# Optimization experiments

Measured on AMD Instinct MI355X. Metric: run time of the kernel, lower is better.

The kernel has to match this reference:

```python
import jax, jax.numpy as jnp
import numpy as np

N = 94  # nodes per graph (pinned by fc = Linear(94, 6400))


def setup_inputs() -> dict:
    key = jax.random.key(0)
    ks = jax.random.split(key, 9)
    B, E = 16384, 1504
    feature = jax.random.normal(ks[0], (B, N, 3), jnp.float32)
    edge_index = jax.random.randint(ks[1], (2, E), 0, N, jnp.int32)
    edge_weight = jax.random.uniform(ks[2], (E,), jnp.float32)
    # GCNConv weights are [in, out] (PyG applies x @ W)
    W1 = jax.random.normal(ks[3], (3, 6), jnp.float32) * 0.5
    b1 = jax.random.normal(ks[4], (6,), jnp.float32) * 0.1
    W2 = jax.random.normal(ks[5], (6, 1), jnp.float32) * 0.5
    b2 = jax.random.normal(ks[6], (1,), jnp.float32) * 0.1
    # nn.Linear stores weight as [out, in]
    Wfc = jax.random.normal(ks[7], (6400, 94), jnp.float32) * 0.1
    bfc = jax.random.normal(ks[8], (6400,), jnp.float32) * 0.1
    return dict(feature=feature, edge_index=edge_index, edge_weight=edge_weight,
                W1=W1, b1=b1, W2=W2, b2=b2, Wfc=Wfc, bfc=bfc)


def _gcn_norm(edge_index, edge_weight):
    # add self-loops with weight 1.0 (PyG default), symmetric normalization
    loops = jnp.arange(N, dtype=edge_index.dtype)
    src = jnp.concatenate([edge_index[0], loops])
    dst = jnp.concatenate([edge_index[1], loops])
    ew = jnp.concatenate([edge_weight, jnp.ones((N,), edge_weight.dtype)])
    deg = jnp.zeros((N,), edge_weight.dtype).at[dst].add(ew)
    dinv = jnp.where(deg > 0, jax.lax.rsqrt(deg), 0.0)
    norm = dinv[src] * ew * dinv[dst]  # [E+N]
    return src, dst, norm


def _gcn_conv(x, W, b, src, dst, norm):
    # x: [B, N, Cin] -> [B, N, Cout]
    xw = x @ W  # [B, N, Cout]
    msgs = xw[:, src, :] * norm[None, :, None]  # gather + scale, [B, E', Cout]
    out = jnp.zeros((x.shape[0], N, W.shape[1]), x.dtype).at[:, dst].add(msgs)
    return out + b


def reference(feature, edge_index, edge_weight, W1, b1, W2, b2, Wfc, bfc):
    src, dst, norm = _gcn_norm(edge_index, edge_weight)
    h = jnp.tanh(_gcn_conv(feature, W1, b1, src, dst, norm))  # [B, N, 6]
    h = jnp.tanh(_gcn_conv(h, W2, b2, src, dst, norm))        # [B, N, 1]
    h = h[..., 0]                                             # squeeze -> [B, N]
    return h @ Wfc.T + bfc                                    # [B, 6400]
```

## Files before the change

### kernel.cpp

```cpp
#include <hip/hip_runtime.h>
#include <hip/hip_bf16.h>
#include <cstddef>

#define NND 94
#define NPAD 96

typedef __attribute__((ext_vector_type(8))) short sh8;
typedef __attribute__((ext_vector_type(4))) float f4v;

__device__ __forceinline__ float ftanh(float x) {
    float e = __expf(2.0f * x);
    return 1.0f - 2.0f / (e + 1.0f);
}

__global__ void k_prep_adj(const int* __restrict__ ei, const float* __restrict__ ew,
                           float* __restrict__ At, int E) {
    __shared__ float deg[NPAD];
    __shared__ float dinv[NPAD];
    int tid = threadIdx.x;
    for (int i = tid; i < NPAD * NPAD; i += blockDim.x) At[i] = 0.0f;
    if (tid < NPAD) deg[tid] = 0.0f;
    __syncthreads();
    for (int e = tid; e < E; e += blockDim.x)
        atomicAdd(&deg[ei[E + e]], ew[e]);
    __syncthreads();
    if (tid < NND) {
        float d = deg[tid] + 1.0f;
        dinv[tid] = d > 0.0f ? rsqrtf(d) : 0.0f;
    }
    __syncthreads();
    for (int e = tid; e < E; e += blockDim.x) {
        int s = ei[e], d = ei[E + e];
        atomicAdd(&At[s * NPAD + d], dinv[s] * ew[e] * dinv[d]);
    }
    if (tid < NND)
        atomicAdd(&At[tid * NPAD + tid], dinv[tid] * dinv[tid]);
}

__global__ void k_pack_w(const float* __restrict__ Wfc, __hip_bfloat16* __restrict__ wp_hi,
                         __hip_bfloat16* __restrict__ wp_lo, int NOUT) {
    int t = blockIdx.x * blockDim.x + threadIdx.x;
    int total = (NOUT / 16) * 3 * 64;
    if (t >= total) return;
    int lane = t & 63;
    int kb = (t >> 6) % 3;
    int ntile = t / 192;
    int n = ntile * 16 + (lane & 15);
    int kbase = kb * 32 + ((lane >> 4) << 3);
    size_t obase = (size_t)t * 8;
#pragma unroll
    for (int j = 0; j < 8; ++j) {
        int k = kbase + j;
        float v = (k < NND) ? Wfc[(size_t)n * NND + k] : 0.0f;
        __hip_bfloat16 h = __float2bfloat16(v);
        float rem = v - __bfloat162float(h);
        wp_hi[obase + j] = h;
        wp_lo[obase + j] = __float2bfloat16(rem);
    }
}

#define K1_THREADS 512
#define NR 12

__global__ void __launch_bounds__(K1_THREADS) k_gcn(
    const float* __restrict__ feat, const float* __restrict__ W1,
    const float* __restrict__ b1, const float* __restrict__ W2,
    const float* __restrict__ b2p, const float* __restrict__ At,
    __hip_bfloat16* __restrict__ h2p) {
    extern __shared__ float lds[];
    float* xs = lds;
    float* zs = lds + 282 * 64;

    int tid = threadIdx.x;
    int lane = tid & 63;
    int g = __builtin_amdgcn_readfirstlane(tid >> 6);
    int b0 = blockIdx.x * 64;

    float w1[3][6], bb1[6], w2[6];
#pragma unroll
    for (int k = 0; k < 3; ++k)
#pragma unroll
        for (int c = 0; c < 6; ++c) w1[k][c] = W1[k * 6 + c];
#pragma unroll
    for (int c = 0; c < 6; ++c) { bb1[c] = b1[c]; w2[c] = W2[c]; }
    float b2 = b2p[0];

    for (int i = tid; i < 282 * 64; i += K1_THREADS) {
        int bl = i & 63;
        int idx = i >> 6;
        xs[idx * 64 + bl] = feat[(size_t)(b0 + bl) * 282 + idx];
    }
    __syncthreads();

    int nb = g * NR;

    float y[NR][3];
#pragma unroll
    for (int i = 0; i < NR; ++i)
#pragma unroll
        for (int k = 0; k < 3; ++k) y[i][k] = 0.0f;

    for (int m = 0; m < NND; ++m) {
        float x0 = xs[(m * 3 + 0) * 64 + lane];
        float x1 = xs[(m * 3 + 1) * 64 + lane];
        float x2 = xs[(m * 3 + 2) * 64 + lane];
        const float* arow = At + m * NPAD + nb;
#pragma unroll
        for (int i = 0; i < NR; ++i) {
            float a = arow[i];
            y[i][0] += a * x0;
            y[i][1] += a * x1;
            y[i][2] += a * x2;
        }
    }

#pragma unroll
    for (int i = 0; i < NR; ++i) {
        int n = nb + i;
        float z = 0.0f;
#pragma unroll
        for (int c = 0; c < 6; ++c) {
            float h = ftanh(y[i][0] * w1[0][c] + y[i][1] * w1[1][c] + y[i][2] * w1[2][c] + bb1[c]);
            z += h * w2[c];
        }
        if (n < NND) zs[n * 64 + lane] = z;
    }
    __syncthreads();

    float s[NR];
#pragma unroll
    for (int i = 0; i < NR; ++i) s[i] = 0.0f;
    for (int m = 0; m < NND; ++m) {
        float zv = zs[m * 64 + lane];
        const float* arow = At + m * NPAD + nb;
#pragma unroll
        for (int i = 0; i < NR; ++i) s[i] += arow[i] * zv;
    }

    int b = b0 + lane;
    int tile = b >> 4;
    int mloc = b & 15;
#pragma unroll
    for (int i = 0; i < NR; ++i) {
        int n = nb + i;
        float h2 = (n < NND) ? ftanh(s[i] + b2) : 0.0f;
        int kb = n >> 5;
        int k32 = n & 31;
        int lp = mloc + ((k32 >> 3) << 4);
        size_t idx = ((size_t)(tile * 3 + kb) * 64 + lp) * 8 + (k32 & 7);
        h2p[idx] = __float2bfloat16(h2);
    }
}

__global__ void __launch_bounds__(256) k_gemm(
    const __hip_bfloat16* __restrict__ h2p, const __hip_bfloat16* __restrict__ wp_hi,
    const __hip_bfloat16* __restrict__ wp_lo, const float* __restrict__ bfc,
    float* __restrict__ out, int NOUT) {
    int tid = threadIdx.x;
    int lane = tid & 63;
    int wid = tid >> 6;
    int nbase = blockIdx.x * 64;
    int mbase = blockIdx.y * 256 + wid * 64;
    int mtile0 = mbase >> 4;
    int ntile0 = nbase >> 4;

    f4v acc[4][4];
#pragma unroll
    for (int mt = 0; mt < 4; ++mt)
#pragma unroll
        for (int nt = 0; nt < 4; ++nt) acc[mt][nt] = (f4v){0.0f, 0.0f, 0.0f, 0.0f};

#pragma unroll
    for (int kb = 0; kb < 3; ++kb) {
        sh8 af[4], bh[4], bl[4];
#pragma unroll
        for (int mt = 0; mt < 4; ++mt)
            af[mt] = *(const sh8*)(h2p + ((size_t)((mtile0 + mt) * 3 + kb) * 64 + lane) * 8);
#pragma unroll
        for (int nt = 0; nt < 4; ++nt) {
            size_t o = ((size_t)((ntile0 + nt) * 3 + kb) * 64 + lane) * 8;
            bh[nt] = *(const sh8*)(wp_hi + o);
            bl[nt] = *(const sh8*)(wp_lo + o);
        }
#pragma unroll
        for (int mt = 0; mt < 4; ++mt)
#pragma unroll
            for (int nt = 0; nt < 4; ++nt) {
                acc[mt][nt] = __builtin_amdgcn_mfma_f32_16x16x32_bf16(af[mt], bh[nt], acc[mt][nt], 0, 0, 0);
                acc[mt][nt] = __builtin_amdgcn_mfma_f32_16x16x32_bf16(af[mt], bl[nt], acc[mt][nt], 0, 0, 0);
            }
    }

    int col0 = lane & 15;
    int rowq = (lane >> 4) * 4;
    float bias[4];
#pragma unroll
    for (int nt = 0; nt < 4; ++nt) bias[nt] = bfc[nbase + nt * 16 + col0];

#pragma unroll
    for (int mt = 0; mt < 4; ++mt) {
#pragma unroll
        for (int r = 0; r < 4; ++r) {
            int row = mbase + mt * 16 + rowq + r;
            float* orow = out + (size_t)row * NOUT + nbase + col0;
#pragma unroll
            for (int nt = 0; nt < 4; ++nt)
                orow[nt * 16] = acc[mt][nt][r] + bias[nt];
        }
    }
}

extern "C" void kernel_launch(void* const* d_in, const int* in_sizes, int n_in,
                              void* d_out, int out_size, void* d_ws, size_t ws_size,
                              hipStream_t stream) {
    const float* feat = (const float*)d_in[0];
    const int*   ei   = (const int*)d_in[1];
    const float* ew   = (const float*)d_in[2];
    const float* W1   = (const float*)d_in[3];
    const float* b1   = (const float*)d_in[4];
    const float* W2   = (const float*)d_in[5];
    const float* b2   = (const float*)d_in[6];
    const float* Wfc  = (const float*)d_in[7];
    const float* bfc  = (const float*)d_in[8];
    float* out = (float*)d_out;

    int E = in_sizes[1] / 2;
    int B = in_sizes[0] / (NND * 3);
    int NOUT = in_sizes[8];

    char* ws = (char*)d_ws;
    float* At = (float*)ws;
    __hip_bfloat16* h2p   = (__hip_bfloat16*)(ws + 40960);
    __hip_bfloat16* wp_hi = (__hip_bfloat16*)(ws + 40960 + 3145728);
    __hip_bfloat16* wp_lo = (__hip_bfloat16*)(ws + 40960 + 3145728 + 1228800);

    k_prep_adj<<<1, 1024, 0, stream>>>(ei, ew, At, E);

    int packT = (NOUT / 16) * 3 * 64;
    k_pack_w<<<(packT + 255) / 256, 256, 0, stream>>>(Wfc, wp_hi, wp_lo, NOUT);

    size_t ldsz = (size_t)(282 * 64 + 94 * 64) * sizeof(float);
    k_gcn<<<B / 64, K1_THREADS, ldsz, stream>>>(feat, W1, b1, W2, b2, At, h2p);

    dim3 g2(NOUT / 64, B / 256);
    k_gemm<<<g2, 256, 0, stream>>>(h2p, wp_hi, wp_lo, bfc, out, NOUT);
}
```

Measured before the change: 498.3 us.

## Pre-transpose features and stage GEMM output through LDS for vectorized stores

Adds a separate transpose kernel so the GCN kernel can load node-major features with coalesced reads instead of strided per-batch gathers. The GEMM epilogue now writes each accumulator tile into shared memory and stores 16-byte vectors per lane, so output rows are written contiguously. The cost is an extra kernel launch and a round trip of the feature tensor through workspace memory, plus extra LDS traffic in the epilogue. The output store of 16384x6400 floats dominates, so the epilogue change is likely the main lever.

```diff
diff --git a/kernel.cpp b/kernel.cpp
--- a/kernel.cpp
+++ b/kernel.cpp
@@ -59,14 +59,36 @@
     }
 }
 
+__global__ void __launch_bounds__(256) k_feat_T(const float* __restrict__ feat,
+                                               float* __restrict__ featT, int B) {
+    __shared__ float tile[64][65];
+    int b0 = blockIdx.x * 64;
+    int c0 = blockIdx.y * 64;
+    int tx = threadIdx.x & 63;
+    int ty = threadIdx.x >> 6;
+#pragma unroll
+    for (int j = 0; j < 16; ++j) {
+        int r = ty + j * 4;
+        int c = c0 + tx;
+        tile[r][tx] = (c < 282) ? feat[(size_t)(b0 + r) * 282 + c] : 0.0f;
+    }
+    __syncthreads();
+#pragma unroll
+    for (int j = 0; j < 16; ++j) {
+        int cc = ty + j * 4;
+        if (c0 + cc < 282)
+            featT[(size_t)(c0 + cc) * B + b0 + tx] = tile[tx][cc];
+    }
+}
+
 #define K1_THREADS 512
 #define NR 12
 
 __global__ void __launch_bounds__(K1_THREADS) k_gcn(
-    const float* __restrict__ feat, const float* __restrict__ W1,
+    const float* __restrict__ featT, const float* __restrict__ W1,
     const float* __restrict__ b1, const float* __restrict__ W2,
     const float* __restrict__ b2p, const float* __restrict__ At,
-    __hip_bfloat16* __restrict__ h2p) {
+    __hip_bfloat16* __restrict__ h2p, int B) {
     extern __shared__ float lds[];
     float* xs = lds;
     float* zs = lds + 282 * 64;
@@ -85,11 +107,8 @@
     for (int c = 0; c < 6; ++c) { bb1[c] = b1[c]; w2[c] = W2[c]; }
     float b2 = b2p[0];
 
-    for (int i = tid; i < 282 * 64; i += K1_THREADS) {
-        int bl = i & 63;
-        int idx = i >> 6;
-        xs[idx * 64 + bl] = feat[(size_t)(b0 + bl) * 282 + idx];
-    }
+    for (int i = tid; i < 282 * 64; i += K1_THREADS)
+        xs[i] = featT[(size_t)(i >> 6) * B + b0 + (i & 63)];
     __syncthreads();
 
     int nb = g * NR;
@@ -156,6 +175,7 @@
     const __hip_bfloat16* __restrict__ h2p, const __hip_bfloat16* __restrict__ wp_hi,
     const __hip_bfloat16* __restrict__ wp_lo, const float* __restrict__ bfc,
     float* __restrict__ out, int NOUT) {
+    __shared__ float tbuf[4][16][68];
     int tid = threadIdx.x;
     int lane = tid & 63;
     int wid = tid >> 6;
@@ -200,12 +220,16 @@
 #pragma unroll
     for (int mt = 0; mt < 4; ++mt) {
 #pragma unroll
-        for (int r = 0; r < 4; ++r) {
-            int row = mbase + mt * 16 + rowq + r;
-            float* orow = out + (size_t)row * NOUT + nbase + col0;
-#pragma unroll
-            for (int nt = 0; nt < 4; ++nt)
-                orow[nt * 16] = acc[mt][nt][r] + bias[nt];
+        for (int nt = 0; nt < 4; ++nt)
+#pragma unroll
+            for (int r = 0; r < 4; ++r)
+                tbuf[wid][rowq + r][nt * 16 + col0] = acc[mt][nt][r] + bias[nt];
+#pragma unroll
+        for (int p = 0; p < 4; ++p) {
+            int rl = p * 4 + (lane >> 4);
+            f4v v = *(const f4v*)&tbuf[wid][rl][col0 * 4];
+            int grow = mbase + mt * 16 + rl;
+            *(f4v*)(out + (size_t)grow * NOUT + nbase + col0 * 4) = v;
         }
     }
 }
@@ -233,14 +257,18 @@
     __hip_bfloat16* h2p   = (__hip_bfloat16*)(ws + 40960);
     __hip_bfloat16* wp_hi = (__hip_bfloat16*)(ws + 40960 + 3145728);
     __hip_bfloat16* wp_lo = (__hip_bfloat16*)(ws + 40960 + 3145728 + 1228800);
+    float* featT = (float*)(ws + 40960 + 3145728 + 2 * 1228800);
 
     k_prep_adj<<<1, 1024, 0, stream>>>(ei, ew, At, E);
 
     int packT = (NOUT / 16) * 3 * 64;
     k_pack_w<<<(packT + 255) / 256, 256, 0, stream>>>(Wfc, wp_hi, wp_lo, NOUT);
 
+    dim3 gT(B / 64, (282 + 63) / 64);
+    k_feat_T<<<gT, 256, 0, stream>>>(feat, featT, B);
+
     size_t ldsz = (size_t)(282 * 64 + 94 * 64) * sizeof(float);
-    k_gcn<<<B / 64, K1_THREADS, ldsz, stream>>>(feat, W1, b1, W2, b2, At, h2p);
+    k_gcn<<<B / 64, K1_THREADS, ldsz, stream>>>(featT, W1, b1, W2, b2, At, h2p, B);
 
     dim3 g2(NOUT / 64, B / 256);
     k_gemm<<<g2, 256, 0, stream>>>(h2p, wp_hi, wp_lo, bfc, out, NOUT);
```

Measured after the change: 510.6 us. 1.02x slower.
